# Performance work log

Hardware: AMD Instinct MI355X
Metric: run time of the kernel (lower is better)

The kernel has to match this reference:

```python
import jax, jax.numpy as jnp
import numpy as np

N = 210          # sequence length (== module max_length cap)
DM = 2048        # input feature dim (major and minor)
DK = 1024        # key/query dim
DV = 1024        # value dim
K_CLIP = 32      # relative-position clipping distance


def _make_table(n, k):
    # table[i, j] = clip(j - i, -k, k) + k  (Shaw-style relative position index)
    rel = np.arange(n)[None, :] - np.arange(n)[:, None]
    return jnp.asarray(np.clip(rel, -k, k) + k, dtype=jnp.int32)


def setup_inputs() -> dict:
    key = jax.random.key(0)
    ks = jax.random.split(key, 7)
    X_major = jax.random.normal(ks[0], (N, DM), dtype=jnp.float32)
    X_minor = jax.random.normal(ks[1], (N, DM), dtype=jnp.float32)
    # Linear weights stored as [in, out] for x @ W
    s = 0.02
    Wq = jax.random.normal(ks[2], (DM, DK), dtype=jnp.float32) * s
    Wk = jax.random.normal(ks[3], (DM, DK), dtype=jnp.float32) * s
    Wv = jax.random.normal(ks[4], (DM, DV), dtype=jnp.float32) * s
    Wo = jax.random.normal(ks[5], (DV, DV), dtype=jnp.float32) * s
    wk = jax.random.normal(ks[6], (2 * K_CLIP + 1, DK), dtype=jnp.float32) * s
    table = _make_table(N, K_CLIP)
    return {"X_major": X_major, "X_minor": X_minor, "Wq": Wq, "Wk": Wk,
            "Wv": Wv, "Wo": Wo, "wk": wk, "table": table}


def reference(X_major, X_minor, Wq, Wk, Wv, Wo, wk, table):
    n = X_major.shape[0]
    scale = 1.0 / jnp.sqrt(jnp.asarray(Wq.shape[1], X_major.dtype))
    Q = X_major @ Wq                     # [n, dk]
    K = X_minor @ Wk                     # [n, dk]
    V = X_minor @ Wv                     # [n, dv]
    Qs = Q * scale
    S = Qs @ K.T                         # [n, n] content scores
    Rk = wk[table[:n, :n]]               # [n, n, dk] gathered rel-pos reps
    Sr = jnp.einsum('id,ijd->ij', Qs, Rk)  # [n, n] relative scores
    A = jax.nn.softmax(S + Sr, axis=-1)  # [n, n]
    Y = (A @ V) @ Wo                     # [n, dv]
    return (Y, A)
```

## Files before the change

### kernel.cpp

```cpp
#include <hip/hip_runtime.h>

typedef short bf16x8 __attribute__((ext_vector_type(8)));
typedef float f32x4 __attribute__((ext_vector_type(4)));

#define MFMA16(a, b, c) __builtin_amdgcn_mfma_f32_16x16x32_bf16(a, b, c, 0, 0, 0)

__device__ inline short f2bf(float f) {
  unsigned u = __builtin_bit_cast(unsigned, f);
  u += 0x7FFFu + ((u >> 16) & 1u);
  return (short)(u >> 16);
}
__device__ inline unsigned pack2(float lo, float hi) {
  unsigned a = __builtin_bit_cast(unsigned, lo) + 0x8000u;
  unsigned b = __builtin_bit_cast(unsigned, hi) + 0x8000u;
  return __builtin_amdgcn_perm(b, a, 0x07060302u);
}
__device__ inline void async_cp16(const void* g, void* l) {
  __builtin_amdgcn_global_load_lds(
      (const __attribute__((address_space(1))) unsigned int*)g,
      (__attribute__((address_space(3))) unsigned int*)l, 16, 0, 0);
}
#define SWZ(r, c) ((((r) << 4) + ((c) ^ ((r) & 7))) << 3)
__device__ inline int swz5(int r, int c) {
  return ((r << 5) + ((c & ~7) | ((c ^ r) & 7))) << 3;
}


__global__ __launch_bounds__(256) void k_prep(const float* __restrict__ xmaj,
                                              const float* __restrict__ xmin,
                                              const float* __restrict__ wkin,
                                              const float* __restrict__ Wq,
                                              const float* __restrict__ Wk,
                                              const float* __restrict__ Wv,
                                              const float* __restrict__ Wo,
                                              short* __restrict__ xmaj_bf,
                                              short* __restrict__ xmin_bf,
                                              short* __restrict__ kwb,
                                              short* __restrict__ wqt,
                                              short* __restrict__ wkt,
                                              short* __restrict__ wvt,
                                              short* __restrict__ wot) {
  __shared__ short tile[64][72];
  int b = blockIdx.x, t = threadIdx.x;
  if (b < 512) {
    int idx = b * 256 + t;
    if (idx < 107520) {
      float4 v = ((const float4*)xmaj)[idx];
      ((uint2*)xmaj_bf)[idx] = make_uint2(pack2(v.x, v.y), pack2(v.z, v.w));
      float4 u = ((const float4*)xmin)[idx];
      ((uint2*)xmin_bf)[idx] = make_uint2(pack2(u.x, u.y), pack2(u.z, u.w));
    }
    if (idx < 16640) {
      float4 v = ((const float4*)wkin)[idx];
      ((uint2*)(kwb + 210 * 1024))[idx] = make_uint2(pack2(v.x, v.y), pack2(v.z, v.w));
    }
    if (idx < 1664) ((uint4*)(kwb + 275 * 1024))[idx] = make_uint4(0, 0, 0, 0);
    return;
  }
  const float* W;
  short* Wt;
  int kt, nt, dstK;
  if (b < 2048) {
    int wi = (b - 512) >> 9, tl = (b - 512) & 511;
    W = wi == 0 ? Wq : (wi == 1 ? Wk : Wv);
    Wt = wi == 0 ? wqt : (wi == 1 ? wkt : wvt);
    kt = tl >> 4; nt = tl & 15; dstK = 2048;
  } else {
    int tl = b - 2048;
    W = Wo; Wt = wot; kt = tl >> 4; nt = tl & 15; dstK = 1024;
  }
  int k0 = kt * 64, n0 = nt * 64;
  int kp = t >> 4, nl4 = (t & 15) * 4;
  for (int h = 0; h < 2; ++h) {
    int kpp = kp + h * 16;
    const float* g = W + (size_t)(k0 + 2 * kpp) * 1024 + n0 + nl4;
    float4 u = *(const float4*)g;
    float4 v = *(const float4*)(g + 1024);
    *(unsigned*)&tile[nl4 + 0][2 * kpp] = pack2(u.x, v.x);
    *(unsigned*)&tile[nl4 + 1][2 * kpp] = pack2(u.y, v.y);
    *(unsigned*)&tile[nl4 + 2][2 * kpp] = pack2(u.z, v.z);
    *(unsigned*)&tile[nl4 + 3][2 * kpp] = pack2(u.w, v.w);
  }
  __syncthreads();
  int nl = t >> 2, cq = t & 3;
  for (int h = 0; h < 2; ++h) {
    int c = cq + h * 4;
    *(uint4*)(Wt + (size_t)(n0 + nl) * dstK + k0 + c * 8) = *(const uint4*)&tile[nl][c * 8];
  }
}

__global__ __launch_bounds__(256, 1) void k_qkv(const short* __restrict__ xmaj,
                                                const short* __restrict__ xmin,
                                                const short* __restrict__ wqt,
                                                const short* __restrict__ wkt,
                                                const short* __restrict__ wvt,
                                                short* __restrict__ qs,
                                                short* __restrict__ kwb,
                                                short* __restrict__ v) {
  __shared__ short As[64 * 128];
  __shared__ short Bs[64 * 128];
  int b = blockIdx.x, t = threadIdx.x;
  int x = b & 7, s = b >> 3;
  int ntile = x * 6 + (s >> 2), mtile = s & 3;
  int nn0 = ntile * 64;
  int mat = nn0 >> 10, ncol0 = nn0 & 1023, m0 = mtile * 64;
  const short* A = (mat == 0) ? xmaj : xmin;
  const short* Bt = (mat == 0) ? wqt : (mat == 1 ? wkt : wvt);
  int lane = t & 63, w = t >> 6;
  int wm = w >> 1, wn = w & 1;
  int l15 = lane & 15, l4 = lane >> 4;
  f32x4 acc[2][2] = {};

  for (int k0 = 0; k0 < 2048; k0 += 128) {
    __syncthreads();
#pragma unroll
    for (int j = 0; j < 4; ++j) {
      int sj = t + j * 256;
      int r = sj >> 4, cg = (sj & 15) ^ (r & 7);
      async_cp16(A + (size_t)(m0 + r) * 2048 + k0 + cg * 8, &As[(w * 64 + j * 256) * 8]);
    }
#pragma unroll
    for (int j = 0; j < 4; ++j) {
      int sj = t + j * 256;
      int r = sj >> 4, cg = (sj & 15) ^ (r & 7);
      async_cp16(Bt + (size_t)(ncol0 + r) * 2048 + k0 + cg * 8, &Bs[(w * 64 + j * 256) * 8]);
    }
    __syncthreads();
#pragma unroll
    for (int kk = 0; kk < 4; ++kk) {
      int c = kk * 4 + l4;
      int ra0 = wm * 32 + l15, ra1 = ra0 + 16;
      int rb0 = wn * 32 + l15, rb1 = rb0 + 16;
      bf16x8 a0 = *(const bf16x8*)&As[SWZ(ra0, c)];
      bf16x8 a1 = *(const bf16x8*)&As[SWZ(ra1, c)];
      bf16x8 b0 = *(const bf16x8*)&Bs[SWZ(rb0, c)];
      bf16x8 b1 = *(const bf16x8*)&Bs[SWZ(rb1, c)];
      acc[0][0] = MFMA16(a0, b0, acc[0][0]);
      acc[0][1] = MFMA16(a0, b1, acc[0][1]);
      acc[1][0] = MFMA16(a1, b0, acc[1][0]);
      acc[1][1] = MFMA16(a1, b1, acc[1][1]);
    }
  }

  float scale = (mat == 0) ? 0.03125f : 1.0f;
  short* dst = (mat == 0) ? qs : (mat == 1 ? kwb : v);
#pragma unroll
  for (int mi = 0; mi < 2; ++mi)
#pragma unroll
    for (int ni = 0; ni < 2; ++ni) {
      int r0 = m0 + wm * 32 + mi * 16 + l4 * 4;
      int c = ncol0 + wn * 32 + ni * 16 + l15;
      for (int j = 0; j < 4; ++j) {
        int r = r0 + j;
        if (r < 210) dst[r * 1024 + c] = f2bf(acc[mi][ni][j] * scale);
      }
    }
}

__global__ __launch_bounds__(256, 1) void k_mid(const short* __restrict__ qs,
                                                const short* __restrict__ kwb,
                                                const short* __restrict__ v,
                                                const short* __restrict__ wot,
                                                float* __restrict__ Sp,
                                                short* __restrict__ vwt) {
  __shared__ short As[2][64 * 128];
  __shared__ short Bs[2][64 * 128];
  int b = blockIdx.x, t = threadIdx.x;
  int lane = t & 63, w = t >> 6;
  int l15 = lane & 15, l4 = lane >> 4;

  if (b < 35) {
    int n0 = (b % 5) * 64, m0 = (b / 5) * 32;
    f32x4 acc[2] = {};
    auto issue = [&](int p) {
      int k0 = p * 128, d = p & 1;
#pragma unroll
      for (int j = 0; j < 2; ++j) {
        int sj = t + j * 256;
        int r = sj >> 4, cg = (sj & 15) ^ (r & 7);
        async_cp16(qs + (size_t)(m0 + r) * 1024 + k0 + cg * 8, &As[d][(j * 256 + w * 64) * 8]);
      }
#pragma unroll
      for (int j = 0; j < 4; ++j) {
        int sj = t + j * 256;
        int r = sj >> 4, cg = (sj & 15) ^ (r & 7);
        async_cp16(kwb + (size_t)(n0 + r) * 1024 + k0 + cg * 8, &Bs[d][(j * 256 + w * 64) * 8]);
      }
    };
    issue(0);
#pragma unroll 1
    for (int p = 0; p < 8; ++p) {
      __syncthreads();
      if (p < 7) issue(p + 1);
      int d = p & 1;
#pragma unroll
      for (int kk = 0; kk < 4; ++kk) {
        int c = kk * 4 + l4;
        bf16x8 a0 = *(const bf16x8*)&As[d][SWZ(l15, c)];
        bf16x8 a1 = *(const bf16x8*)&As[d][SWZ(16 + l15, c)];
        bf16x8 bb = *(const bf16x8*)&Bs[d][SWZ(w * 16 + l15, c)];
        acc[0] = MFMA16(a0, bb, acc[0]);
        acc[1] = MFMA16(a1, bb, acc[1]);
      }
    }
#pragma unroll
    for (int mi = 0; mi < 2; ++mi) {
      int r0 = m0 + mi * 16 + l4 * 4;
      int col = n0 + w * 16 + l15;
      for (int j = 0; j < 4; ++j) Sp[(r0 + j) * 320 + col] = acc[mi][j];
    }
  } else {
    int bb = b - 35;
    int n0 = (bb & 15) * 64, m0 = (bb >> 4) * 64;
    int wm = w >> 1, wn = w & 1;
    f32x4 acc[2][2] = {};
    auto issue = [&](int p) {
      int k0 = p * 128, d = p & 1;
#pragma unroll
      for (int j = 0; j < 4; ++j) {
        int sj = t + j * 256;
        int r = sj >> 4, cg = (sj & 15) ^ (r & 7);
        async_cp16(v + (size_t)(m0 + r) * 1024 + k0 + cg * 8, &As[d][(j * 256 + w * 64) * 8]);
        async_cp16(wot + (size_t)(n0 + r) * 1024 + k0 + cg * 8, &Bs[d][(j * 256 + w * 64) * 8]);
      }
    };
    issue(0);
#pragma unroll 1
    for (int p = 0; p < 8; ++p) {
      __syncthreads();
      if (p < 7) issue(p + 1);
      int d = p & 1;
#pragma unroll
      for (int kk = 0; kk < 4; ++kk) {
        int c = kk * 4 + l4;
        int ra0 = wm * 32 + l15, ra1 = ra0 + 16;
        int rb0 = wn * 32 + l15, rb1 = rb0 + 16;
        bf16x8 a0 = *(const bf16x8*)&As[d][SWZ(ra0, c)];
        bf16x8 a1 = *(const bf16x8*)&As[d][SWZ(ra1, c)];
        bf16x8 b0 = *(const bf16x8*)&Bs[d][SWZ(rb0, c)];
        bf16x8 b1 = *(const bf16x8*)&Bs[d][SWZ(rb1, c)];
        acc[0][0] = MFMA16(a0, b0, acc[0][0]);
        acc[0][1] = MFMA16(a0, b1, acc[0][1]);
        acc[1][0] = MFMA16(a1, b0, acc[1][0]);
        acc[1][1] = MFMA16(a1, b1, acc[1][1]);
      }
    }
    __syncthreads();
    short* scr = &As[0][0];
#pragma unroll
    for (int mi = 0; mi < 2; ++mi)
#pragma unroll
      for (int ni = 0; ni < 2; ++ni) {
        int nl = wn * 32 + ni * 16 + l15;
        int ml0 = wm * 32 + mi * 16 + l4 * 4;
        for (int j = 0; j < 4; ++j) scr[nl * 72 + ml0 + j] = f2bf(acc[mi][ni][j]);
      }
    __syncthreads();
    for (int h = 0; h < 2; ++h) {
      int idx = t + h * 256;
      int nl = idx >> 3, c8 = idx & 7;
      int mg0 = m0 + c8 * 8;
      short* dstp = vwt + (size_t)(n0 + nl) * 256 + mg0;
      if (mg0 + 8 <= 210) {
        *(uint4*)dstp = *(const uint4*)&scr[nl * 72 + c8 * 8];
      } else {
        for (int e = 0; e < 8; ++e)
          if (mg0 + e < 210) dstp[e] = scr[nl * 72 + c8 * 8 + e];
      }
    }
  }
}

__global__ __launch_bounds__(256) void k_softmax(const float* __restrict__ Sp,
                                                 const int* __restrict__ table,
                                                 short* __restrict__ Abf,
                                                 float* __restrict__ outA) {
  int i = blockIdx.x, t = threadIdx.x;
  if (i >= 210) {
    Abf[i * 256 + t] = 0;
    return;
  }
  __shared__ float srow[288];
  __shared__ float red[4];
  for (int j = t; j < 288; j += 256) srow[j] = Sp[i * 320 + j];
  __syncthreads();
  float logit = -1e30f;
  if (t < 210) {
    int tb = table[i * 210 + t];
    logit = srow[t] + srow[210 + tb];
  }
  float m = logit;
  for (int o = 32; o; o >>= 1) m = fmaxf(m, __shfl_xor(m, o));
  if ((t & 63) == 0) red[t >> 6] = m;
  __syncthreads();
  m = fmaxf(fmaxf(red[0], red[1]), fmaxf(red[2], red[3]));
  float e = (t < 210) ? __expf(logit - m) : 0.0f;
  float s = e;
  for (int o = 32; o; o >>= 1) s += __shfl_xor(s, o);
  __syncthreads();
  if ((t & 63) == 0) red[t >> 6] = s;
  __syncthreads();
  s = red[0] + red[1] + red[2] + red[3];
  float a = e / s;
  Abf[i * 256 + t] = (t < 210) ? f2bf(a) : (short)0;
  if (t < 210) outA[i * 210 + t] = a;
}

__global__ __launch_bounds__(256, 1) void k_fin(const short* __restrict__ Abf,
                                                const short* __restrict__ vwt,
                                                float* __restrict__ outY) {
  __shared__ short As[64 * 256];
  __shared__ short Bs[64 * 256];
  int n0 = blockIdx.x * 64, m0 = blockIdx.y * 64;
  int t = threadIdx.x, lane = t & 63, w = t >> 6;
  int wm = w >> 1, wn = w & 1;
  int l15 = lane & 15, l4 = lane >> 4;

#pragma unroll
  for (int j = 0; j < 8; ++j) {
    int sj = t + j * 256;
    int r = sj >> 5, c = sj & 31;
    int cg = (c & ~7) | ((c ^ r) & 7);
    async_cp16(Abf + (size_t)(m0 + r) * 256 + cg * 8, &As[(j * 256 + w * 64) * 8]);
    async_cp16(vwt + (size_t)(n0 + r) * 256 + cg * 8, &Bs[(j * 256 + w * 64) * 8]);
  }
  __syncthreads();

  f32x4 acc[2][2] = {};
#pragma unroll
  for (int kk = 0; kk < 8; ++kk) {
    int c = kk * 4 + l4;
    int ra0 = wm * 32 + l15, ra1 = ra0 + 16;
    int rb0 = wn * 32 + l15, rb1 = rb0 + 16;
    bf16x8 a0 = *(const bf16x8*)&As[swz5(ra0, c)];
    bf16x8 a1 = *(const bf16x8*)&As[swz5(ra1, c)];
    bf16x8 b0 = *(const bf16x8*)&Bs[swz5(rb0, c)];
    bf16x8 b1 = *(const bf16x8*)&Bs[swz5(rb1, c)];
    acc[0][0] = MFMA16(a0, b0, acc[0][0]);
    acc[0][1] = MFMA16(a0, b1, acc[0][1]);
    acc[1][0] = MFMA16(a1, b0, acc[1][0]);
    acc[1][1] = MFMA16(a1, b1, acc[1][1]);
  }
#pragma unroll
  for (int mi = 0; mi < 2; ++mi)
#pragma unroll
    for (int ni = 0; ni < 2; ++ni) {
      int r0 = m0 + wm * 32 + mi * 16 + l4 * 4;
      int c = n0 + wn * 32 + ni * 16 + l15;
      for (int j = 0; j < 4; ++j) {
        int r = r0 + j;
        if (r < 210) outY[r * 1024 + c] = acc[mi][ni][j];
      }
    }
}

extern "C" void kernel_launch(void* const* d_in, const int* in_sizes, int n_in,
                              void* d_out, int out_size, void* d_ws, size_t ws_size,
                              hipStream_t stream) {
  const float* Xmaj = (const float*)d_in[0];
  const float* Xmin = (const float*)d_in[1];
  const float* Wq = (const float*)d_in[2];
  const float* Wk = (const float*)d_in[3];
  const float* Wv = (const float*)d_in[4];
  const float* Wo = (const float*)d_in[5];
  const float* wk = (const float*)d_in[6];
  const int* table = (const int*)d_in[7];

  char* ws = (char*)d_ws;
  short* xmaj_bf = (short*)(ws + 0);
  short* xmin_bf = (short*)(ws + 1048576);
  short* qs = (short*)(ws + 2097152);
  short* kwb = (short*)(ws + 2621440);
  short* vwt = (short*)(ws + 3276800);
  short* Abf = (short*)(ws + 3801088);
  short* v = (short*)(ws + 3932160);
  float* Sp = (float*)(ws + 4456448);
  short* wqt = (short*)(ws + 4743168);
  short* wkt = (short*)(ws + 8937472);
  short* wvt = (short*)(ws + 13131776);
  short* wot = (short*)(ws + 17326080);

  float* outY = (float*)d_out;
  float* outA = (float*)d_out + 215040;

  k_prep<<<2304, 256, 0, stream>>>(Xmaj, Xmin, wk, Wq, Wk, Wv, Wo,
                                   xmaj_bf, xmin_bf, kwb, wqt, wkt, wvt, wot);
  k_qkv<<<192, 256, 0, stream>>>(xmaj_bf, xmin_bf, wqt, wkt, wvt, qs, kwb, v);
  k_mid<<<99, 256, 0, stream>>>(qs, kwb, v, wot, Sp, vwt);
  k_softmax<<<256, 256, 0, stream>>>(Sp, table, Abf, outA);
  k_fin<<<dim3(16, 4), 256, 0, stream>>>(Abf, vwt, outY);
}
```

Baseline: 120.8 us.

## Fuse softmax into final A·(VWo) GEMM kernel, drop separate softmax launch

Removes the standalone softmax kernel. Each k_fin block now loads its 64 rows of raw score partials into LDS, computes the relative-position logits from a clip of j-i rather than the table, and runs the softmax. It writes the bf16 probabilities straight into the GEMM A tile, and the blocks with n0==0 also write outA. This saves one launch and the bf16 A round trip through global memory. In exchange, the softmax is recomputed redundantly across the 16 column blocks, and the larger LDS footprint (about 139 KB) may limit occupancy.

Result: slower. 133.3 us (+10.3%).

```diff
diff --git a/kernel.cpp b/kernel.cpp
--- a/kernel.cpp
+++ b/kernel.cpp
@@ -271,46 +271,13 @@
   }
 }
 
-__global__ __launch_bounds__(256) void k_softmax(const float* __restrict__ Sp,
-                                                 const int* __restrict__ table,
-                                                 short* __restrict__ Abf,
-                                                 float* __restrict__ outA) {
-  int i = blockIdx.x, t = threadIdx.x;
-  if (i >= 210) {
-    Abf[i * 256 + t] = 0;
-    return;
-  }
-  __shared__ float srow[288];
-  __shared__ float red[4];
-  for (int j = t; j < 288; j += 256) srow[j] = Sp[i * 320 + j];
-  __syncthreads();
-  float logit = -1e30f;
-  if (t < 210) {
-    int tb = table[i * 210 + t];
-    logit = srow[t] + srow[210 + tb];
-  }
-  float m = logit;
-  for (int o = 32; o; o >>= 1) m = fmaxf(m, __shfl_xor(m, o));
-  if ((t & 63) == 0) red[t >> 6] = m;
-  __syncthreads();
-  m = fmaxf(fmaxf(red[0], red[1]), fmaxf(red[2], red[3]));
-  float e = (t < 210) ? __expf(logit - m) : 0.0f;
-  float s = e;
-  for (int o = 32; o; o >>= 1) s += __shfl_xor(s, o);
-  __syncthreads();
-  if ((t & 63) == 0) red[t >> 6] = s;
-  __syncthreads();
-  s = red[0] + red[1] + red[2] + red[3];
-  float a = e / s;
-  Abf[i * 256 + t] = (t < 210) ? f2bf(a) : (short)0;
-  if (t < 210) outA[i * 210 + t] = a;
-}
-
-__global__ __launch_bounds__(256, 1) void k_fin(const short* __restrict__ Abf,
+__global__ __launch_bounds__(256, 1) void k_fin(const float* __restrict__ Sp,
                                                 const short* __restrict__ vwt,
-                                                float* __restrict__ outY) {
+                                                float* __restrict__ outY,
+                                                float* __restrict__ outA) {
   __shared__ short As[64 * 256];
   __shared__ short Bs[64 * 256];
+  __shared__ float Ss[64 * 292];
   int n0 = blockIdx.x * 64, m0 = blockIdx.y * 64;
   int t = threadIdx.x, lane = t & 63, w = t >> 6;
   int wm = w >> 1, wn = w & 1;
@@ -321,8 +288,47 @@
     int sj = t + j * 256;
     int r = sj >> 5, c = sj & 31;
     int cg = (c & ~7) | ((c ^ r) & 7);
-    async_cp16(Abf + (size_t)(m0 + r) * 256 + cg * 8, &As[(j * 256 + w * 64) * 8]);
     async_cp16(vwt + (size_t)(n0 + r) * 256 + cg * 8, &Bs[(j * 256 + w * 64) * 8]);
+  }
+  for (int i = t; i < 4608; i += 256) {
+    int r = i / 72, c4 = i % 72;
+    int src = m0 + r;
+    src = src > 209 ? 209 : src;
+    *(float4*)&Ss[r * 292 + c4 * 4] = *(const float4*)(Sp + (size_t)src * 320 + c4 * 4);
+  }
+  __syncthreads();
+
+  {
+    int r = t >> 2, q = t & 3;
+    int grow = m0 + r;
+    float* Sr = Ss + r * 292;
+    float mx = -1e30f;
+    for (int j = q; j < 210; j += 4) {
+      int d = j - grow;
+      d = d < -32 ? -32 : (d > 32 ? 32 : d);
+      mx = fmaxf(mx, Sr[j] + Sr[242 + d]);
+    }
+    for (int o = 2; o; o >>= 1) mx = fmaxf(mx, __shfl_xor(mx, o, 4));
+    float sum = 0.0f;
+    for (int j = q; j < 210; j += 4) {
+      int d = j - grow;
+      d = d < -32 ? -32 : (d > 32 ? 32 : d);
+      float e = __expf(Sr[j] + Sr[242 + d] - mx);
+      Sr[j] = e;
+      sum += e;
+    }
+    for (int o = 2; o; o >>= 1) sum += __shfl_xor(sum, o, 4);
+    float inv = 1.0f / sum;
+    bool wA = (n0 == 0) && (grow < 210);
+    for (int j = q; j < 256; j += 4) {
+      if (j < 210) {
+        float a = Sr[j] * inv;
+        As[swz5(r, j >> 3) + (j & 7)] = f2bf(a);
+        if (wA) outA[(size_t)grow * 210 + j] = a;
+      } else {
+        As[swz5(r, j >> 3) + (j & 7)] = 0;
+      }
+    }
   }
   __syncthreads();
 
@@ -364,7 +370,6 @@
   const float* Wv = (const float*)d_in[4];
   const float* Wo = (const float*)d_in[5];
   const float* wk = (const float*)d_in[6];
-  const int* table = (const int*)d_in[7];
 
   char* ws = (char*)d_ws;
   short* xmaj_bf = (short*)(ws + 0);
@@ -372,7 +377,6 @@
   short* qs = (short*)(ws + 2097152);
   short* kwb = (short*)(ws + 2621440);
   short* vwt = (short*)(ws + 3276800);
-  short* Abf = (short*)(ws + 3801088);
   short* v = (short*)(ws + 3932160);
   float* Sp = (float*)(ws + 4456448);
   short* wqt = (short*)(ws + 4743168);
@@ -387,6 +391,5 @@
                                    xmaj_bf, xmin_bf, kwb, wqt, wkt, wvt, wot);
   k_qkv<<<192, 256, 0, stream>>>(xmaj_bf, xmin_bf, wqt, wkt, wvt, qs, kwb, v);
   k_mid<<<99, 256, 0, stream>>>(qs, kwb, v, wot, Sp, vwt);
-  k_softmax<<<256, 256, 0, stream>>>(Sp, table, Abf, outA);
-  k_fin<<<dim3(16, 4), 256, 0, stream>>>(Abf, vwt, outY);
-}
+  k_fin<<<dim3(16, 4), 256, 0, stream>>>(Sp, vwt, outY, outA);
+}
```
